# Kernel tuning notes

Measured on AMD Instinct MI355X. Metric: run time of the kernel, lower is better.

Reference implementation:

```python
import jax, jax.numpy as jnp
import numpy as np

NQ = 11          # qubits per atom
NL = 3           # circuit layers (and message-passing layers)
S = 2 ** NQ      # statevector size
PAD = 100        # feature-map input width


def setup_inputs() -> dict:
    key = jax.random.key(0)
    ks = jax.random.split(key, 18)
    B, A, F, E = 8, 96, 64, 384
    return {
        "node_features": jax.random.normal(ks[0], (B, A, F), jnp.float32),
        "edge_indices": jax.random.randint(ks[1], (2, E), 0, A),
        # QuantumFeatureMap.feature_preprocessor: Linear(100,64) -> ReLU -> Linear(64,NQ) -> Tanh
        "W1": jax.random.normal(ks[2], (64, PAD), jnp.float32) * 0.1,
        "b1": jnp.zeros((64,), jnp.float32),
        "W2": jax.random.normal(ks[3], (NQ, 64), jnp.float32) * 0.1,
        "b2": jnp.zeros((NQ,), jnp.float32),
        # QuantumFeatureMap circuit params
        "rot": jax.random.normal(ks[4], (NL, NQ, 3), jnp.float32),
        "ent": jax.random.normal(ks[5], (NL, NQ - 1), jnp.float32),
        # one QuantumMessagePassing layer per NL, each with message_gates [NQ,3]
        "msg_gates": jax.random.normal(ks[6], (NL, NQ, 3), jnp.float32),
        # QuantumGlobalPooling
        "pool_w": jax.random.normal(ks[7], (NQ,), jnp.float32),
        # output MLP: Linear(2*NQ,256)->ReLU->Linear(256,128)->ReLU->Linear(128,64)
        "Wo1": jax.random.normal(ks[8], (256, 2 * NQ), jnp.float32) * 0.1,
        "bo1": jnp.zeros((256,), jnp.float32),
        "Wo2": jax.random.normal(ks[9], (128, 256), jnp.float32) * 0.05,
        "bo2": jnp.zeros((128,), jnp.float32),
        "Wo3": jax.random.normal(ks[10], (64, 128), jnp.float32) * 0.05,
        "bo3": jnp.zeros((64,), jnp.float32),
    }


def _apply_rotation(amps, M, q):
    """Apply per-batch 2x2 gate M [N,2,2] on qubit q of amps [N,S]."""
    N = amps.shape[0]
    lo = 1 << q
    hi = S // (2 * lo)
    a = amps.reshape(N, hi, 2, lo)  # bit q of state index is the middle axis
    return jnp.einsum('nij,nhjl->nhil', M, a).reshape(N, S)


def _forward(node_features, W1, b1, W2, b2, rot, ent, msg_gates, pool_w,
             Wo1, bo1, Wo2, bo2, Wo3, bo3):
    B, A, F = node_features.shape
    N = B * A
    # --- QuantumNodeEmbedding: pad atom features to 100, shared feature map ---
    x = node_features.reshape(N, F)
    x = jnp.pad(x, ((0, 0), (0, PAD - F)))
    h = jax.nn.relu(x @ W1.T + b1)
    f = jnp.tanh(h @ W2.T + b2)            # [N, NQ] per-qubit angles scaling
    amps = jnp.zeros((N, S), jnp.complex64).at[:, 0].set(1.0)
    states = jnp.arange(S)
    # --- QuantumFeatureMap circuit ---
    for l in range(NL):
        for q in range(NQ):
            rx = rot[l, q, 0] * f[:, q]
            ry = rot[l, q, 1] * f[:, q]
            rz = rot[l, q, 2] * f[:, q]
            cx, sx = jnp.cos(rx / 2), jnp.sin(rx / 2)
            cy, sy = jnp.cos(ry / 2), jnp.sin(ry / 2)
            cz, sz = jnp.cos(rz / 2), jnp.sin(rz / 2)
            # rotation matrix exactly as in the torch source
            M = jnp.stack([cx * cy * cz, -sx * sy * sz,
                           sx * sy * cz,  cx * cy * sz], -1)
            M = M.reshape(N, 2, 2).astype(jnp.complex64)
            amps = _apply_rotation(amps, M, q)
        for q in range(NQ - 1):
            # parameterized CNOT: for control-bit==1, mix state with target-flipped partner
            p = jax.nn.sigmoid(ent[l, q]).astype(jnp.complex64)
            ctrl = (states >> q) & 1
            partner = states ^ (1 << (q + 1))
            mixed = (1 - p) * amps + p * amps[:, partner]
            amps = jnp.where(ctrl[None, :] == 1, mixed, amps)
    # --- QuantumMessagePassing layers: diagonal phase exp(i*sum(theta_q over set bits)) ---
    bits = ((states[:, None] >> jnp.arange(NQ)[None, :]) & 1).astype(jnp.float32)  # [S,NQ]
    for l in range(NL):
        theta = msg_gates[l].sum(-1)                 # [NQ] rx+ry+rz per qubit
        phase = jnp.exp(1j * (bits @ theta))         # [S] complex64
        amps = amps * phase[None, :]
    # --- QuantumGlobalPooling ---
    amps_b = amps.reshape(B, A, S)
    w = jax.nn.sigmoid(pool_w[jnp.arange(A) % NQ]).astype(jnp.complex64)  # atom i -> w[i%NQ]
    pooled = jnp.einsum('a,bas->bs', w, amps_b)      # [B,S] complex
    norm = jnp.sqrt(jnp.sum(pooled.real ** 2 + pooled.imag ** 2, axis=1, keepdims=True))
    pooled = pooled / jnp.maximum(norm, 1e-12)
    rm = jnp.tile(pooled.real.mean(1, keepdims=True), (1, NQ))
    im = jnp.tile(pooled.imag.mean(1, keepdims=True), (1, NQ))
    rep = jnp.concatenate([rm, im], axis=1)          # [B, 2*NQ]
    # --- output network ---
    h1 = jax.nn.relu(rep @ Wo1.T + bo1)
    h2 = jax.nn.relu(h1 @ Wo2.T + bo2)
    return h2 @ Wo3.T + bo3                          # [B, 64]


def reference(node_features, edge_indices, W1, b1, W2, b2, rot, ent, msg_gates,
              pool_w, Wo1, bo1, Wo2, bo2, Wo3, bo3):
    # edge_indices is accepted by the torch module but does not enter the math
    del edge_indices
    return _forward(node_features, W1, b1, W2, b2, rot, ent, msg_gates, pool_w,
                    Wo1, bo1, Wo2, bo2, Wo3, bo3)
```

## Files before the change

kernel.cpp:

```cpp
#include <hip/hip_runtime.h>

#define NQ 11
#define NL 3
#define S  2048
#define NB 8
#define NA 96
#define NF 64
#define PADW 100
#define WPB 4

__device__ __forceinline__ float sigmoidf_(float x) { return 1.0f / (1.0f + expf(-x)); }

__global__ __launch_bounds__(256) void circuit_kernel(
    const float* __restrict__ nf,
    const float* __restrict__ W1,
    const float* __restrict__ b1,
    const float* __restrict__ W2,
    const float* __restrict__ b2,
    const float* __restrict__ rot,
    const float* __restrict__ ent,
    const float* __restrict__ pool_w,
    float* __restrict__ Racc)
{
    __shared__ float W1s[64 * 65];
    __shared__ float xs[WPB][64];

    const int tid   = threadIdx.x;
    const int lane  = tid & 63;
    const int wave  = tid >> 6;
    const int node0 = blockIdx.x * WPB;
    const int node  = node0 + wave;
    const int b     = node / NA;
    const int a     = node % NA;

    {
        const int r  = tid >> 2;
        const int c0 = (tid & 3) << 4;
        const float4* src = reinterpret_cast<const float4*>(W1 + r * PADW + c0);
        float* dst = &W1s[r * 65 + c0];
#pragma unroll
        for (int j = 0; j < 4; ++j) {
            const float4 vv = src[j];
            dst[4 * j + 0] = vv.x; dst[4 * j + 1] = vv.y;
            dst[4 * j + 2] = vv.z; dst[4 * j + 3] = vv.w;
        }
        xs[wave][lane] = nf[node0 * NF + tid];
    }
    __syncthreads();

    float h = b1[lane];
    {
        const float* wrow = &W1s[lane * 65];
        const float* xv   = xs[wave];
#pragma unroll
        for (int k = 0; k < 64; ++k) h = fmaf(wrow[k], xv[k], h);
    }
    h = fmaxf(h, 0.0f);

    float fscal = 0.0f;
#pragma unroll
    for (int q = 0; q < NQ; ++q) {
        float t = h * W2[q * 64 + lane];
#pragma unroll
        for (int off = 32; off >= 1; off >>= 1) t += __shfl_xor(t, off, 64);
        if (lane == q) fscal = tanhf(t + b2[q]);
    }

    const int qidx = lane < 11 ? lane : (lane < 22 ? lane - 11 : (lane < 33 ? lane - 22 : 0));
    const float fg = __shfl(fscal, qidx, 64);
    float m00 = 0.f, m01 = 0.f, m10 = 0.f, m11 = 0.f;
    if (lane < NL * NQ) {
        const float* r = rot + lane * 3;
        const float hx = 0.5f * r[0] * fg;
        const float hy = 0.5f * r[1] * fg;
        const float hz = 0.5f * r[2] * fg;
        const float cx = cosf(hx), sx = sinf(hx);
        const float cy = cosf(hy), sy = sinf(hy);
        const float cz = cosf(hz), sz = sinf(hz);
        m00 = cx * cy * cz; m01 = -sx * sy * sz;
        m10 = sx * sy * cz; m11 = cx * cy * sz;
    }
    float pent = 0.0f;
    if (lane < NL * (NQ - 1)) pent = sigmoidf_(ent[lane]);

    float v[32];
#pragma unroll
    for (int i = 0; i < 32; ++i) v[i] = 0.0f;
    if (lane == 0) v[0] = 1.0f;

    for (int l = 0; l < NL; ++l) {
#pragma unroll
        for (int q = 0; q < NQ; ++q) {
            const int g = l * NQ + q;
            const float g00 = __shfl(m00, g, 64);
            const float g01 = __shfl(m01, g, 64);
            const float g10 = __shfl(m10, g, 64);
            const float g11 = __shfl(m11, g, 64);
            if (q < 6) {
                const int   bit = (lane >> q) & 1;
                const float c0  = bit ? g10 : g01;
                const float c1  = bit ? g11 : g00;
#pragma unroll
                for (int i = 0; i < 32; ++i) {
                    const float pv = __shfl_xor(v[i], 1 << q, 64);
                    v[i] = fmaf(c0, pv, c1 * v[i]);
                }
            } else {
                const int rb = 1 << (q - 6);
#pragma unroll
                for (int j = 0; j < 16; ++j) {
                    const int i0 = ((j >> (q - 6)) << (q - 5)) | (j & (rb - 1));
                    const int i1 = i0 | rb;
                    const float a0 = v[i0], a1 = v[i1];
                    v[i0] = fmaf(g00, a0, g01 * a1);
                    v[i1] = fmaf(g10, a0, g11 * a1);
                }
            }
        }
#pragma unroll
        for (int q = 0; q < NQ - 1; ++q) {
            const float p = __shfl(pent, l * (NQ - 1) + q, 64);
            if (q < 5) {
                const int act = (lane >> q) & 1;
#pragma unroll
                for (int i = 0; i < 32; ++i) {
                    const float pv = __shfl_xor(v[i], 1 << (q + 1), 64);
                    const float nv = fmaf(p, pv - v[i], v[i]);
                    v[i] = act ? nv : v[i];
                }
            } else if (q == 5) {
                const int act = (lane >> 5) & 1;
#pragma unroll
                for (int j = 0; j < 16; ++j) {
                    const int i0 = 2 * j, i1 = 2 * j + 1;
                    const float d   = v[i1] - v[i0];
                    const float nv0 = fmaf(p, d, v[i0]);
                    const float nv1 = fmaf(-p, d, v[i1]);
                    v[i0] = act ? nv0 : v[i0];
                    v[i1] = act ? nv1 : v[i1];
                }
            } else {
                const int cb = q - 6;
#pragma unroll
                for (int j = 0; j < 8; ++j) {
                    const int i0 = ((j >> cb) << (cb + 2)) | (1 << cb) | (j & ((1 << cb) - 1));
                    const int i1 = i0 | (1 << (cb + 1));
                    const float d = v[i1] - v[i0];
                    v[i0] = fmaf(p, d, v[i0]);
                    v[i1] = fmaf(-p, d, v[i1]);
                }
            }
        }
    }

    const float w = sigmoidf_(pool_w[a % NQ]);
    float* Rb = Racc + b * S;
#pragma unroll
    for (int i = 0; i < 32; ++i)
        atomicAdd(&Rb[(i << 6) | lane], w * v[i]);
}

__global__ __launch_bounds__(256) void pool_mlp_kernel(
    const float* __restrict__ Racc,
    const float* __restrict__ msg,
    const float* __restrict__ Wo1, const float* __restrict__ bo1,
    const float* __restrict__ Wo2, const float* __restrict__ bo2,
    const float* __restrict__ Wo3, const float* __restrict__ bo3,
    float* __restrict__ out)
{
    __shared__ float Theta[NQ];
    __shared__ float red[3][4];
    __shared__ float rm_sh, im_sh;
    __shared__ float h1[256];
    __shared__ float h2[128];

    const int b   = blockIdx.x;
    const int tid = threadIdx.x;

    if (tid < NQ) {
        float t = 0.0f;
        for (int l = 0; l < NL; ++l)
#pragma unroll
            for (int c = 0; c < 3; ++c) t += msg[(l * NQ + tid) * 3 + c];
        Theta[tid] = t;
    }
    __syncthreads();

    float psq = 0.0f, pc = 0.0f, ps = 0.0f;
    const float* Rb = Racc + b * S;
    for (int s = tid; s < S; s += 256) {
        const float R = Rb[s];
        float phi = 0.0f;
#pragma unroll
        for (int q = 0; q < NQ; ++q)
            if ((s >> q) & 1) phi += Theta[q];
        psq += R * R;
        pc  += R * cosf(phi);
        ps  += R * sinf(phi);
    }
#pragma unroll
    for (int off = 32; off >= 1; off >>= 1) {
        psq += __shfl_down(psq, off, 64);
        pc  += __shfl_down(pc,  off, 64);
        ps  += __shfl_down(ps,  off, 64);
    }
    const int lane = tid & 63, wave = tid >> 6;
    if (lane == 0) { red[0][wave] = psq; red[1][wave] = pc; red[2][wave] = ps; }
    __syncthreads();
    if (tid == 0) {
        const float sq = red[0][0] + red[0][1] + red[0][2] + red[0][3];
        const float sc = red[1][0] + red[1][1] + red[1][2] + red[1][3];
        const float ss = red[2][0] + red[2][1] + red[2][2] + red[2][3];
        const float norm = fmaxf(sqrtf(sq), 1e-12f);
        rm_sh = sc / (float)S / norm;
        im_sh = ss / (float)S / norm;
    }
    __syncthreads();
    const float rm = rm_sh, im = im_sh;

    {
        float s1 = 0.0f, s2 = 0.0f;
        const float* wrow = Wo1 + tid * (2 * NQ);
#pragma unroll
        for (int k = 0; k < NQ; ++k)       s1 += wrow[k];
#pragma unroll
        for (int k = NQ; k < 2 * NQ; ++k)  s2 += wrow[k];
        h1[tid] = fmaxf(rm * s1 + im * s2 + bo1[tid], 0.0f);
    }
    __syncthreads();
    if (tid < 128) {
        float acc = bo2[tid];
        const float* wrow = Wo2 + tid * 256;
        for (int k = 0; k < 256; ++k) acc += h1[k] * wrow[k];
        h2[tid] = fmaxf(acc, 0.0f);
    }
    __syncthreads();
    if (tid < 64) {
        float acc = bo3[tid];
        const float* wrow = Wo3 + tid * 128;
        for (int k = 0; k < 128; ++k) acc += h2[k] * wrow[k];
        out[b * 64 + tid] = acc;
    }
}

extern "C" void kernel_launch(void* const* d_in, const int* in_sizes, int n_in,
                              void* d_out, int out_size, void* d_ws, size_t ws_size,
                              hipStream_t stream) {
    const float* nf     = (const float*)d_in[0];
    const float* W1     = (const float*)d_in[2];
    const float* b1     = (const float*)d_in[3];
    const float* W2     = (const float*)d_in[4];
    const float* b2     = (const float*)d_in[5];
    const float* rot    = (const float*)d_in[6];
    const float* ent    = (const float*)d_in[7];
    const float* msg    = (const float*)d_in[8];
    const float* pool_w = (const float*)d_in[9];
    const float* Wo1    = (const float*)d_in[10];
    const float* bo1    = (const float*)d_in[11];
    const float* Wo2    = (const float*)d_in[12];
    const float* bo2    = (const float*)d_in[13];
    const float* Wo3    = (const float*)d_in[14];
    const float* bo3    = (const float*)d_in[15];

    float* Racc = (float*)d_ws;
    hipMemsetAsync(Racc, 0, NB * S * sizeof(float), stream);

    circuit_kernel<<<dim3(NB * NA / WPB), dim3(256), 0, stream>>>(
        nf, W1, b1, W2, b2, rot, ent, pool_w, Racc);

    pool_mlp_kernel<<<dim3(NB), dim3(256), 0, stream>>>(
        Racc, msg, Wo1, bo1, Wo2, bo2, Wo3, bo3, (float*)d_out);
}
```

Measured before the change: 124.8 us.

## Replace global atomics with per-block partial sums and drop memset

Each circuit block now reduces its four waves' weighted statevectors in shared memory and writes one partial vector per block. The pooling kernel sums the 24 partials per batch using 1024 threads, so the global atomicAdd traffic and the hipMemsetAsync launch go away. Entangler select operations are also replaced by multiplying the angle by a 0/1 mask. The cost is 32KB of extra shared memory per circuit block, which may reduce occupancy, and extra partial-buffer reads in the pooling kernel.

```diff
diff --git a/kernel.cpp b/kernel.cpp
--- a/kernel.cpp
+++ b/kernel.cpp
@@ -8,6 +8,7 @@
 #define NF 64
 #define PADW 100
 #define WPB 4
+#define PPB (NA / WPB)
 
 __device__ __forceinline__ float sigmoidf_(float x) { return 1.0f / (1.0f + expf(-x)); }
 
@@ -20,17 +21,17 @@
     const float* __restrict__ rot,
     const float* __restrict__ ent,
     const float* __restrict__ pool_w,
-    float* __restrict__ Racc)
+    float* __restrict__ Rpart)
 {
     __shared__ float W1s[64 * 65];
     __shared__ float xs[WPB][64];
+    __shared__ float psum[WPB][S];
 
     const int tid   = threadIdx.x;
     const int lane  = tid & 63;
     const int wave  = tid >> 6;
     const int node0 = blockIdx.x * WPB;
     const int node  = node0 + wave;
-    const int b     = node / NA;
     const int a     = node % NA;
 
     {
@@ -121,23 +122,20 @@
         for (int q = 0; q < NQ - 1; ++q) {
             const float p = __shfl(pent, l * (NQ - 1) + q, 64);
             if (q < 5) {
-                const int act = (lane >> q) & 1;
+                const float pact = p * (float)((lane >> q) & 1);
 #pragma unroll
                 for (int i = 0; i < 32; ++i) {
                     const float pv = __shfl_xor(v[i], 1 << (q + 1), 64);
-                    const float nv = fmaf(p, pv - v[i], v[i]);
-                    v[i] = act ? nv : v[i];
+                    v[i] = fmaf(pact, pv - v[i], v[i]);
                 }
             } else if (q == 5) {
-                const int act = (lane >> 5) & 1;
+                const float pact = p * (float)((lane >> 5) & 1);
 #pragma unroll
                 for (int j = 0; j < 16; ++j) {
                     const int i0 = 2 * j, i1 = 2 * j + 1;
-                    const float d   = v[i1] - v[i0];
-                    const float nv0 = fmaf(p, d, v[i0]);
-                    const float nv1 = fmaf(-p, d, v[i1]);
-                    v[i0] = act ? nv0 : v[i0];
-                    v[i1] = act ? nv1 : v[i1];
+                    const float d = v[i1] - v[i0];
+                    v[i0] = fmaf(pact, d, v[i0]);
+                    v[i1] = fmaf(-pact, d, v[i1]);
                 }
             } else {
                 const int cb = q - 6;
@@ -154,14 +152,16 @@
     }
 
     const float w = sigmoidf_(pool_w[a % NQ]);
-    float* Rb = Racc + b * S;
-#pragma unroll
-    for (int i = 0; i < 32; ++i)
-        atomicAdd(&Rb[(i << 6) | lane], w * v[i]);
+#pragma unroll
+    for (int i = 0; i < 32; ++i) psum[wave][(i << 6) | lane] = w * v[i];
+    __syncthreads();
+    float* Rb = Rpart + blockIdx.x * S;
+    for (int s = tid; s < S; s += 256)
+        Rb[s] = psum[0][s] + psum[1][s] + psum[2][s] + psum[3][s];
 }
 
-__global__ __launch_bounds__(256) void pool_mlp_kernel(
-    const float* __restrict__ Racc,
+__global__ __launch_bounds__(1024) void pool_mlp_kernel(
+    const float* __restrict__ Rpart,
     const float* __restrict__ msg,
     const float* __restrict__ Wo1, const float* __restrict__ bo1,
     const float* __restrict__ Wo2, const float* __restrict__ bo2,
@@ -169,7 +169,7 @@
     float* __restrict__ out)
 {
     __shared__ float Theta[NQ];
-    __shared__ float red[3][4];
+    __shared__ float red[3][16];
     __shared__ float rm_sh, im_sh;
     __shared__ float h1[256];
     __shared__ float h2[128];
@@ -187,9 +187,11 @@
     __syncthreads();
 
     float psq = 0.0f, pc = 0.0f, ps = 0.0f;
-    const float* Rb = Racc + b * S;
-    for (int s = tid; s < S; s += 256) {
-        const float R = Rb[s];
+    const float* Pb = Rpart + b * PPB * S;
+    for (int s = tid; s < S; s += 1024) {
+        float R = 0.0f;
+#pragma unroll
+        for (int j = 0; j < PPB; ++j) R += Pb[j * S + s];
         float phi = 0.0f;
 #pragma unroll
         for (int q = 0; q < NQ; ++q)
@@ -200,17 +202,17 @@
     }
 #pragma unroll
     for (int off = 32; off >= 1; off >>= 1) {
-        psq += __shfl_down(psq, off, 64);
-        pc  += __shfl_down(pc,  off, 64);
-        ps  += __shfl_down(ps,  off, 64);
+        psq += __shfl_xor(psq, off, 64);
+        pc  += __shfl_xor(pc,  off, 64);
+        ps  += __shfl_xor(ps,  off, 64);
     }
     const int lane = tid & 63, wave = tid >> 6;
     if (lane == 0) { red[0][wave] = psq; red[1][wave] = pc; red[2][wave] = ps; }
     __syncthreads();
     if (tid == 0) {
-        const float sq = red[0][0] + red[0][1] + red[0][2] + red[0][3];
-        const float sc = red[1][0] + red[1][1] + red[1][2] + red[1][3];
-        const float ss = red[2][0] + red[2][1] + red[2][2] + red[2][3];
+        float sq = 0.f, sc = 0.f, ss = 0.f;
+#pragma unroll
+        for (int wv = 0; wv < 16; ++wv) { sq += red[0][wv]; sc += red[1][wv]; ss += red[2][wv]; }
         const float norm = fmaxf(sqrtf(sq), 1e-12f);
         rm_sh = sc / (float)S / norm;
         im_sh = ss / (float)S / norm;
@@ -218,7 +220,7 @@
     __syncthreads();
     const float rm = rm_sh, im = im_sh;
 
-    {
+    if (tid < 256) {
         float s1 = 0.0f, s2 = 0.0f;
         const float* wrow = Wo1 + tid * (2 * NQ);
 #pragma unroll
@@ -262,12 +264,11 @@
     const float* Wo3    = (const float*)d_in[14];
     const float* bo3    = (const float*)d_in[15];
 
-    float* Racc = (float*)d_ws;
-    hipMemsetAsync(Racc, 0, NB * S * sizeof(float), stream);
+    float* Rpart = (float*)d_ws;
 
     circuit_kernel<<<dim3(NB * NA / WPB), dim3(256), 0, stream>>>(
-        nf, W1, b1, W2, b2, rot, ent, pool_w, Racc);
-
-    pool_mlp_kernel<<<dim3(NB), dim3(256), 0, stream>>>(
-        Racc, msg, Wo1, bo1, Wo2, bo2, Wo3, bo3, (float*)d_out);
+        nf, W1, b1, W2, b2, rot, ent, pool_w, Rpart);
+
+    pool_mlp_kernel<<<dim3(NB), dim3(1024), 0, stream>>>(
+        Rpart, msg, Wo1, bo1, Wo2, bo2, Wo3, bo3, (float*)d_out);
 }
```

Measured after the change: 123.0 us. Within noise of the previous version (-1.5%).
